# Performance work log

Measured on AMD Instinct MI355X. Metric: run time of the kernel, lower is better.

## Reference

```python
import jax, jax.numpy as jnp
import numpy as np

B, N, D, F = 8, 2048, 768, 768

def setup_inputs() -> dict:
    key = jax.random.key(0)
    k1, k2, k3, k4 = jax.random.split(key, 4)
    inputs = jax.random.normal(k1, (B, N, D), dtype=jnp.float32)
    # keras 'uniform' initializer: RandomUniform(-0.05, 0.05)
    W_q = jax.random.uniform(k2, (D, F), dtype=jnp.float32, minval=-0.05, maxval=0.05)
    W_k = jax.random.uniform(k3, (D, F), dtype=jnp.float32, minval=-0.05, maxval=0.05)
    W_v = jax.random.uniform(k4, (D, D), dtype=jnp.float32, minval=-0.05, maxval=0.05)
    return {"inputs": inputs, "W_q": W_q, "W_k": W_k, "W_v": W_v}

def reference(inputs, W_q, W_k, W_v):
    # q,k: [B,N,F]; v: [B,N,D]
    q = jnp.einsum('bnd,df->bnf', inputs, W_q)
    k = jnp.einsum('bnd,df->bnf', inputs, W_k)
    v = jnp.einsum('bnd,de->bne', inputs, W_v)
    scores = jnp.einsum('bnf,bmf->bnm', q, k)  # [B,N,N], no 1/sqrt(d) scaling (as in source)
    attn = jax.nn.softmax(scores, axis=-1)
    out = jnp.einsum('bnm,bmd->bnd', attn, v)
    return out
```

## Files before the change

### kernel.cpp

```cpp
#include <hip/hip_runtime.h>


typedef __attribute__((ext_vector_type(8))) _Float16 half8;
typedef __attribute__((ext_vector_type(4))) _Float16 half4v;
typedef __attribute__((ext_vector_type(4))) float floatx4;

__device__ __forceinline__ _Float16 f2h(float f) { return (_Float16)f; }
#define MFMA16 __builtin_amdgcn_mfma_f32_16x16x32_f16

__global__ __launch_bounds__(256) void cast_x_kernel(const float* __restrict__ X,
    _Float16* __restrict__ Xh) {
  size_t idx = (size_t)blockIdx.x * 256 + threadIdx.x;
  for (size_t o8 = idx; o8 < 1572864u; o8 += 524288u) {
    size_t o = o8 * 8;
    float4 a = *(const float4*)(X + o);
    float4 b = *(const float4*)(X + o + 4);
    *(half8*)(Xh + o) = (half8){f2h(a.x), f2h(a.y), f2h(a.z), f2h(a.w),
                                f2h(b.x), f2h(b.y), f2h(b.z), f2h(b.w)};
  }
}

__global__ __launch_bounds__(256) void mm_small_kernel(const float* __restrict__ Wq,
    const float* __restrict__ Wk, _Float16* __restrict__ Mh) {
  __shared__ _Float16 As[128][72];
  __shared__ _Float16 Bs[128][72];
  int bn = blockIdx.x, bm = blockIdx.y;
  int tid = threadIdx.x, lane = tid & 63, wave = tid >> 6;
  int wm = wave >> 1, wn = wave & 1;
  int l15 = lane & 15, quad = lane >> 4;
  floatx4 acc[16];
  for (int i = 0; i < 16; i++) acc[i] = (floatx4){0.f, 0.f, 0.f, 0.f};
  for (int k0 = 0; k0 < 768; k0 += 64) {
    __syncthreads();
    for (int i = 0; i < 8; i++) {
      int f = i * 256 + tid;
      int row = f >> 4, c4 = (f & 15) << 2;
      float4 va = *(const float4*)(Wq + (size_t)(bm * 128 + row) * 768 + k0 + c4);
      *(half4v*)&As[row][c4] = (half4v){f2h(va.x), f2h(va.y), f2h(va.z), f2h(va.w)};
      float4 vb = *(const float4*)(Wk + (size_t)(bn * 128 + row) * 768 + k0 + c4);
      *(half4v*)&Bs[row][c4] = (half4v){f2h(vb.x), f2h(vb.y), f2h(vb.z), f2h(vb.w)};
    }
    __syncthreads();
    for (int kk = 0; kk < 2; kk++) {
      half8 a[4], b[4];
      for (int mt = 0; mt < 4; mt++) a[mt] = *(half8*)&As[wm * 64 + mt * 16 + l15][kk * 32 + quad * 8];
      for (int nt = 0; nt < 4; nt++) b[nt] = *(half8*)&Bs[wn * 64 + nt * 16 + l15][kk * 32 + quad * 8];
      for (int mt = 0; mt < 4; mt++)
        for (int nt = 0; nt < 4; nt++)
          acc[mt * 4 + nt] = MFMA16(a[mt], b[nt], acc[mt * 4 + nt], 0, 0, 0);
    }
  }
  for (int mt = 0; mt < 4; mt++)
    for (int nt = 0; nt < 4; nt++) {
      int e = bn * 128 + wn * 64 + nt * 16 + l15;
      for (int r = 0; r < 4; r++) {
        int d = bm * 128 + wm * 64 + mt * 16 + quad * 4 + r;
        Mh[(size_t)d * 768 + e] = f2h(acc[mt * 4 + nt][r]);
      }
    }
}

__global__ void pack_wv_kernel(const float* __restrict__ Wv, _Float16* __restrict__ WvT) {
  __shared__ float tile[32][33];
  int k0 = blockIdx.x * 32;
  int n0 = blockIdx.y * 32;
  int tx = threadIdx.x, ty = threadIdx.y;
  for (int yy = ty; yy < 32; yy += 8)
    tile[yy][tx] = Wv[(size_t)(k0 + yy) * 768 + n0 + tx];
  __syncthreads();
  for (int yy = ty; yy < 32; yy += 8)
    WvT[(size_t)(n0 + yy) * 768 + k0 + tx] = f2h(tile[tx][yy]);
}

__global__ __launch_bounds__(256) void proj_h_kernel(const _Float16* __restrict__ Xh,
    const _Float16* __restrict__ Mh, _Float16* __restrict__ H) {
  __shared__ _Float16 As[128][72];
  __shared__ _Float16 Bs[128][72];
  int bn = blockIdx.x, bm = blockIdx.y;
  int tid = threadIdx.x, lane = tid & 63, wave = tid >> 6;
  int wm = wave >> 1, wn = wave & 1;
  int l15 = lane & 15, quad = lane >> 4;
  floatx4 acc[16];
  for (int i = 0; i < 16; i++) acc[i] = (floatx4){0.f, 0.f, 0.f, 0.f};
  for (int k0 = 0; k0 < 768; k0 += 64) {
    __syncthreads();
    for (int i = 0; i < 4; i++) {
      int f = i * 256 + tid;
      int row = f >> 3, c8 = (f & 7) << 3;
      *(half8*)&As[row][c8] = *(const half8*)(Xh + (size_t)(bm * 128 + row) * 768 + k0 + c8);
      *(half8*)&Bs[row][c8] = *(const half8*)(Mh + (size_t)(bn * 128 + row) * 768 + k0 + c8);
    }
    __syncthreads();
    for (int kk = 0; kk < 2; kk++) {
      half8 a[4], b[4];
      for (int mt = 0; mt < 4; mt++) a[mt] = *(half8*)&As[wm * 64 + mt * 16 + l15][kk * 32 + quad * 8];
      for (int nt = 0; nt < 4; nt++) b[nt] = *(half8*)&Bs[wn * 64 + nt * 16 + l15][kk * 32 + quad * 8];
      for (int mt = 0; mt < 4; mt++)
        for (int nt = 0; nt < 4; nt++)
          acc[mt * 4 + nt] = MFMA16(a[mt], b[nt], acc[mt * 4 + nt], 0, 0, 0);
    }
  }
  for (int mt = 0; mt < 4; mt++)
    for (int nt = 0; nt < 4; nt++) {
      int col = bn * 128 + wn * 64 + nt * 16 + l15;
      for (int r = 0; r < 4; r++) {
        int row = bm * 128 + wm * 64 + mt * 16 + quad * 4 + r;
        H[(size_t)row * 768 + col] = f2h(acc[mt * 4 + nt][r]);
      }
    }
}

__global__ __launch_bounds__(256) void proj_v_kernel(const _Float16* __restrict__ Xh,
    const _Float16* __restrict__ WvT, _Float16* __restrict__ Vt) {
  __shared__ _Float16 As[128][72];
  __shared__ _Float16 Bs[128][72];
  int bn = blockIdx.x, bm = blockIdx.y;
  int tid = threadIdx.x, lane = tid & 63, wave = tid >> 6;
  int wm = wave >> 1, wn = wave & 1;
  int l15 = lane & 15, quad = lane >> 4;
  floatx4 acc[16];
  for (int i = 0; i < 16; i++) acc[i] = (floatx4){0.f, 0.f, 0.f, 0.f};
  for (int k0 = 0; k0 < 768; k0 += 64) {
    __syncthreads();
    for (int i = 0; i < 4; i++) {
      int f = i * 256 + tid;
      int row = f >> 3, c8 = (f & 7) << 3;
      *(half8*)&As[row][c8] = *(const half8*)(Xh + (size_t)(bm * 128 + row) * 768 + k0 + c8);
      *(half8*)&Bs[row][c8] = *(const half8*)(WvT + (size_t)(bn * 128 + row) * 768 + k0 + c8);
    }
    __syncthreads();
    for (int kk = 0; kk < 2; kk++) {
      half8 a[4], b[4];
      for (int mt = 0; mt < 4; mt++) a[mt] = *(half8*)&As[wm * 64 + mt * 16 + l15][kk * 32 + quad * 8];
      for (int nt = 0; nt < 4; nt++) b[nt] = *(half8*)&Bs[wn * 64 + nt * 16 + l15][kk * 32 + quad * 8];
      for (int mt = 0; mt < 4; mt++)
        for (int nt = 0; nt < 4; nt++)
          acc[mt * 4 + nt] = MFMA16(a[mt], b[nt], acc[mt * 4 + nt], 0, 0, 0);
    }
  }
  for (int mt = 0; mt < 4; mt++)
    for (int nt = 0; nt < 4; nt++) {
      int d = bn * 128 + wn * 64 + nt * 16 + l15;
      int tok0 = bm * 128 + wm * 64 + mt * 16 + quad * 4;
      int bb = tok0 >> 11, ntok = tok0 & 2047;
      half4v p;
      for (int r = 0; r < 4; r++) p[r] = f2h(acc[mt * 4 + nt][r]);
      *(half4v*)(Vt + (size_t)(bb * 768 + d) * 2048 + ntok) = p;
    }
}

__global__ __launch_bounds__(512, 2) void attn_kernel(const _Float16* __restrict__ H,
    const float* __restrict__ X, const _Float16* __restrict__ Vt, float* __restrict__ out) {
  __shared__ _Float16 Qs[64][776];
  __shared__ _Float16 Pl[64][136];
  __shared__ float pm[8][64];
  __shared__ float psum[8][64];
  __shared__ float m_run[64], l_run[64], gmax[64], galpha[64];

  int id = blockIdx.x;
  int b = id & 7;
  int q0 = (id >> 3) * 64;
  int tid = threadIdx.x;
  int lane = tid & 63, w = tid >> 6;
  int l15 = lane & 15, quad = lane >> 4;

  if (tid < 64) { m_run[tid] = -1e30f; l_run[tid] = 0.f; }

  floatx4 accO[24];
  for (int i = 0; i < 24; i++) accO[i] = (floatx4){0.f, 0.f, 0.f, 0.f};

  const float*    Xq    = X + (size_t)(b * 2048 + q0) * 768;
  const _Float16* Hbase = H + (size_t)(b * 2048) * 768;
  const _Float16* Vbase = Vt + (size_t)b * 768 * 2048;

  for (int i = 0; i < 12; i++) {
    int f = i * 512 + tid;
    int row = f / 96, c8 = (f % 96) * 8;
    float4 a = *(const float4*)(Xq + (size_t)row * 768 + c8);
    float4 c = *(const float4*)(Xq + (size_t)row * 768 + c8 + 4);
    *(half8*)&Qs[row][c8] = (half8){f2h(a.x), f2h(a.y), f2h(a.z), f2h(a.w),
                                    f2h(c.x), f2h(c.y), f2h(c.z), f2h(c.w)};
  }
  __syncthreads();

  for (int m0 = 0; m0 < 2048; m0 += 128) {
    floatx4 sa[4];
    #pragma unroll
    for (int ss = 0; ss < 4; ss++) sa[ss] = (floatx4){0.f, 0.f, 0.f, 0.f};
    const _Float16* Kr = Hbase + (size_t)(m0 + w * 16 + l15) * 768 + quad * 8;
    half8 kpre[8];
    #pragma unroll
    for (int i = 0; i < 8; i++) kpre[i] = *(const half8*)(Kr + i * 32);
    #pragma unroll
    for (int kb = 0; kb < 24; kb++) {
      half8 kcur = kpre[kb & 7];
      int nxt = (kb + 8 < 24) ? (kb + 8) * 32 : 0;
      kpre[kb & 7] = *(const half8*)(Kr + nxt);
      #pragma unroll
      for (int ss = 0; ss < 4; ss++) {
        half8 qa = *(half8*)&Qs[ss * 16 + l15][kb * 32 + quad * 8];
        sa[ss] = MFMA16(qa, kcur, sa[ss], 0, 0, 0);
      }
    }
    const _Float16* vb0 = Vbase + (size_t)(w * 96 + l15) * 2048 + m0 + quad * 8;
    half8 vpre[8];
    #pragma unroll
    for (int i = 0; i < 8; i++) {
      int nks = i / 6, nnt = i % 6;
      vpre[i] = *(const half8*)(vb0 + (size_t)nnt * 16 * 2048 + nks * 32);
    }

    float mv[16];
    #pragma unroll
    for (int i = 0; i < 16; i++) mv[i] = sa[i >> 2][i & 3];
    #pragma unroll
    for (int mask = 1; mask <= 8; mask <<= 1)
      #pragma unroll
      for (int i = 0; i < 16; i++) mv[i] = fmaxf(mv[i], __shfl_xor(mv[i], mask));
    if (l15 == 0) {
      #pragma unroll
      for (int i = 0; i < 16; i++) pm[w][(i >> 2) * 16 + quad * 4 + (i & 3)] = mv[i];
    }
    __syncthreads();
    if (tid < 64) {
      float mo = m_run[tid];
      float mn = mo;
      #pragma unroll
      for (int w2 = 0; w2 < 8; w2++) mn = fmaxf(mn, pm[w2][tid]);
      gmax[tid] = mn;
      galpha[tid] = __expf(mo - mn);
      m_run[tid] = mn;
    }
    __syncthreads();
    float pr[16], al[16];
    #pragma unroll
    for (int i = 0; i < 16; i++) {
      int ss = i >> 2, r = i & 3;
      int row = ss * 16 + quad * 4 + r;
      float mn = gmax[row];
      al[i] = galpha[row];
      float p = __expf(sa[ss][r] - mn);
      pr[i] = p;
      Pl[row][w * 16 + l15] = f2h(p);
    }
    #pragma unroll
    for (int mask = 1; mask <= 8; mask <<= 1)
      #pragma unroll
      for (int i = 0; i < 16; i++) pr[i] += __shfl_xor(pr[i], mask);
    if (l15 == 0) {
      #pragma unroll
      for (int i = 0; i < 16; i++) psum[w][(i >> 2) * 16 + quad * 4 + (i & 3)] = pr[i];
    }
    #pragma unroll
    for (int nt = 0; nt < 6; nt++)
      #pragma unroll
      for (int i = 0; i < 16; i++)
        accO[nt * 4 + (i >> 2)][i & 3] *= al[i];
    __syncthreads();
    if (tid < 64) {
      float s = 0.f;
      #pragma unroll
      for (int w2 = 0; w2 < 8; w2++) s += psum[w2][tid];
      l_run[tid] = l_run[tid] * galpha[tid] + s;
    }
    #pragma unroll
    for (int ks = 0; ks < 4; ks++) {
      half8 pa[4];
      #pragma unroll
      for (int ss = 0; ss < 4; ss++) pa[ss] = *(half8*)&Pl[ss * 16 + l15][ks * 32 + quad * 8];
      #pragma unroll
      for (int nt = 0; nt < 6; nt++) {
        int idx = ks * 6 + nt;
        half8 vcur = vpre[idx & 7];
        int nidx = idx + 8;
        int nks = (nidx < 24) ? nidx / 6 : 0;
        int nnt = (nidx < 24) ? nidx % 6 : 0;
        vpre[idx & 7] = *(const half8*)(vb0 + (size_t)nnt * 16 * 2048 + nks * 32);
        #pragma unroll
        for (int ss = 0; ss < 4; ss++)
          accO[nt * 4 + ss] = MFMA16(pa[ss], vcur, accO[nt * 4 + ss], 0, 0, 0);
      }
    }
  }
  __syncthreads();
  float il[16];
  #pragma unroll
  for (int i = 0; i < 16; i++) {
    int row = (i >> 2) * 16 + quad * 4 + (i & 3);
    il[i] = 1.f / l_run[row];
  }
  #pragma unroll
  for (int nt = 0; nt < 6; nt++)
    #pragma unroll
    for (int ss = 0; ss < 4; ss++) {
      int d = w * 96 + nt * 16 + l15;
      #pragma unroll
      for (int r = 0; r < 4; r++) {
        int row = q0 + ss * 16 + quad * 4 + r;
        out[(size_t)(b * 2048 + row) * 768 + d] = accO[nt * 4 + ss][r] * il[ss * 4 + r];
      }
    }
}

extern "C" void kernel_launch(void* const* d_in, const int* in_sizes, int n_in,
                              void* d_out, int out_size, void* d_ws, size_t ws_size,
                              hipStream_t stream) {
  (void)in_sizes; (void)n_in; (void)out_size; (void)ws_size;
  const float* X  = (const float*)d_in[0];
  const float* Wq = (const float*)d_in[1];
  const float* Wk = (const float*)d_in[2];
  const float* Wv = (const float*)d_in[3];
  float* out = (float*)d_out;

  char* ws = (char*)d_ws;
  _Float16* H  = (_Float16*)ws;
  _Float16* Vt = (_Float16*)(ws + 25165824);

  _Float16* Mh  = (_Float16*)d_out;
  _Float16* WvT = (_Float16*)((char*)d_out + 2359296);
  _Float16* Xh  = (_Float16*)((char*)d_out + 4194304);

  cast_x_kernel<<<2048, 256, 0, stream>>>(X, Xh);
  mm_small_kernel<<<dim3(6, 6), 256, 0, stream>>>(Wq, Wk, Mh);
  pack_wv_kernel<<<dim3(24, 24), dim3(32, 8), 0, stream>>>(Wv, WvT);
  proj_h_kernel<<<dim3(6, 128), 256, 0, stream>>>(Xh, Mh, H);
  proj_v_kernel<<<dim3(6, 128), 256, 0, stream>>>(Xh, WvT, Vt);
  attn_kernel<<<256, 512, 0, stream>>>(H, X, Vt, out);
}
```

Baseline: 447.7 us.

## Double-buffer projection GEMM tiles and prefetch next K/V block in attention

The two projection GEMMs now stage their tiles through a pair of shared-memory buffers, loading the next K-slice from global memory into registers while MFMAs run on the current one, which cuts one barrier per iteration. In the attention kernel, the K and V register prefetch rings now reach across block boundaries: the tail prefetches pull the first chunks of the next 128-key block rather than reloading the current one, and the prologue loads are hoisted out of the loop. The aim is to hide global load latency at block starts. The cost is twice the LDS in the projection kernels and some redundant wrap-around loads on the last block.

```diff
diff --git a/kernel.cpp b/kernel.cpp
--- a/kernel.cpp
+++ b/kernel.cpp
@@ -74,30 +74,61 @@
 
 __global__ __launch_bounds__(256) void proj_h_kernel(const _Float16* __restrict__ Xh,
     const _Float16* __restrict__ Mh, _Float16* __restrict__ H) {
-  __shared__ _Float16 As[128][72];
-  __shared__ _Float16 Bs[128][72];
+  __shared__ _Float16 As[2][128][72];
+  __shared__ _Float16 Bs[2][128][72];
   int bn = blockIdx.x, bm = blockIdx.y;
   int tid = threadIdx.x, lane = tid & 63, wave = tid >> 6;
   int wm = wave >> 1, wn = wave & 1;
   int l15 = lane & 15, quad = lane >> 4;
   floatx4 acc[16];
   for (int i = 0; i < 16; i++) acc[i] = (floatx4){0.f, 0.f, 0.f, 0.f};
-  for (int k0 = 0; k0 < 768; k0 += 64) {
-    __syncthreads();
-    for (int i = 0; i < 4; i++) {
-      int f = i * 256 + tid;
-      int row = f >> 3, c8 = (f & 7) << 3;
-      *(half8*)&As[row][c8] = *(const half8*)(Xh + (size_t)(bm * 128 + row) * 768 + k0 + c8);
-      *(half8*)&Bs[row][c8] = *(const half8*)(Mh + (size_t)(bn * 128 + row) * 768 + k0 + c8);
-    }
-    __syncthreads();
+  half8 ra[4], rb[4];
+  #pragma unroll
+  for (int i = 0; i < 4; i++) {
+    int f = i * 256 + tid, row = f >> 3, c8 = (f & 7) << 3;
+    ra[i] = *(const half8*)(Xh + (size_t)(bm * 128 + row) * 768 + c8);
+    rb[i] = *(const half8*)(Mh + (size_t)(bn * 128 + row) * 768 + c8);
+  }
+  #pragma unroll
+  for (int i = 0; i < 4; i++) {
+    int f = i * 256 + tid, row = f >> 3, c8 = (f & 7) << 3;
+    *(half8*)&As[0][row][c8] = ra[i];
+    *(half8*)&Bs[0][row][c8] = rb[i];
+  }
+  __syncthreads();
+  int cur = 0;
+  for (int t = 0; t < 12; t++) {
+    if (t < 11) {
+      int k0 = (t + 1) * 64;
+      #pragma unroll
+      for (int i = 0; i < 4; i++) {
+        int f = i * 256 + tid, row = f >> 3, c8 = (f & 7) << 3;
+        ra[i] = *(const half8*)(Xh + (size_t)(bm * 128 + row) * 768 + k0 + c8);
+        rb[i] = *(const half8*)(Mh + (size_t)(bn * 128 + row) * 768 + k0 + c8);
+      }
+    }
+    #pragma unroll
     for (int kk = 0; kk < 2; kk++) {
       half8 a[4], b[4];
-      for (int mt = 0; mt < 4; mt++) a[mt] = *(half8*)&As[wm * 64 + mt * 16 + l15][kk * 32 + quad * 8];
-      for (int nt = 0; nt < 4; nt++) b[nt] = *(half8*)&Bs[wn * 64 + nt * 16 + l15][kk * 32 + quad * 8];
+      #pragma unroll
+      for (int mt = 0; mt < 4; mt++) a[mt] = *(half8*)&As[cur][wm * 64 + mt * 16 + l15][kk * 32 + quad * 8];
+      #pragma unroll
+      for (int nt = 0; nt < 4; nt++) b[nt] = *(half8*)&Bs[cur][wn * 64 + nt * 16 + l15][kk * 32 + quad * 8];
+      #pragma unroll
       for (int mt = 0; mt < 4; mt++)
+        #pragma unroll
         for (int nt = 0; nt < 4; nt++)
           acc[mt * 4 + nt] = MFMA16(a[mt], b[nt], acc[mt * 4 + nt], 0, 0, 0);
+    }
+    if (t < 11) {
+      #pragma unroll
+      for (int i = 0; i < 4; i++) {
+        int f = i * 256 + tid, row = f >> 3, c8 = (f & 7) << 3;
+        *(half8*)&As[cur ^ 1][row][c8] = ra[i];
+        *(half8*)&Bs[cur ^ 1][row][c8] = rb[i];
+      }
+      __syncthreads();
+      cur ^= 1;
     }
   }
   for (int mt = 0; mt < 4; mt++)
@@ -112,30 +143,61 @@
 
 __global__ __launch_bounds__(256) void proj_v_kernel(const _Float16* __restrict__ Xh,
     const _Float16* __restrict__ WvT, _Float16* __restrict__ Vt) {
-  __shared__ _Float16 As[128][72];
-  __shared__ _Float16 Bs[128][72];
+  __shared__ _Float16 As[2][128][72];
+  __shared__ _Float16 Bs[2][128][72];
   int bn = blockIdx.x, bm = blockIdx.y;
   int tid = threadIdx.x, lane = tid & 63, wave = tid >> 6;
   int wm = wave >> 1, wn = wave & 1;
   int l15 = lane & 15, quad = lane >> 4;
   floatx4 acc[16];
   for (int i = 0; i < 16; i++) acc[i] = (floatx4){0.f, 0.f, 0.f, 0.f};
-  for (int k0 = 0; k0 < 768; k0 += 64) {
-    __syncthreads();
-    for (int i = 0; i < 4; i++) {
-      int f = i * 256 + tid;
-      int row = f >> 3, c8 = (f & 7) << 3;
-      *(half8*)&As[row][c8] = *(const half8*)(Xh + (size_t)(bm * 128 + row) * 768 + k0 + c8);
-      *(half8*)&Bs[row][c8] = *(const half8*)(WvT + (size_t)(bn * 128 + row) * 768 + k0 + c8);
-    }
-    __syncthreads();
+  half8 ra[4], rb[4];
+  #pragma unroll
+  for (int i = 0; i < 4; i++) {
+    int f = i * 256 + tid, row = f >> 3, c8 = (f & 7) << 3;
+    ra[i] = *(const half8*)(Xh + (size_t)(bm * 128 + row) * 768 + c8);
+    rb[i] = *(const half8*)(WvT + (size_t)(bn * 128 + row) * 768 + c8);
+  }
+  #pragma unroll
+  for (int i = 0; i < 4; i++) {
+    int f = i * 256 + tid, row = f >> 3, c8 = (f & 7) << 3;
+    *(half8*)&As[0][row][c8] = ra[i];
+    *(half8*)&Bs[0][row][c8] = rb[i];
+  }
+  __syncthreads();
+  int cur = 0;
+  for (int t = 0; t < 12; t++) {
+    if (t < 11) {
+      int k0 = (t + 1) * 64;
+      #pragma unroll
+      for (int i = 0; i < 4; i++) {
+        int f = i * 256 + tid, row = f >> 3, c8 = (f & 7) << 3;
+        ra[i] = *(const half8*)(Xh + (size_t)(bm * 128 + row) * 768 + k0 + c8);
+        rb[i] = *(const half8*)(WvT + (size_t)(bn * 128 + row) * 768 + k0 + c8);
+      }
+    }
+    #pragma unroll
     for (int kk = 0; kk < 2; kk++) {
       half8 a[4], b[4];
-      for (int mt = 0; mt < 4; mt++) a[mt] = *(half8*)&As[wm * 64 + mt * 16 + l15][kk * 32 + quad * 8];
-      for (int nt = 0; nt < 4; nt++) b[nt] = *(half8*)&Bs[wn * 64 + nt * 16 + l15][kk * 32 + quad * 8];
+      #pragma unroll
+      for (int mt = 0; mt < 4; mt++) a[mt] = *(half8*)&As[cur][wm * 64 + mt * 16 + l15][kk * 32 + quad * 8];
+      #pragma unroll
+      for (int nt = 0; nt < 4; nt++) b[nt] = *(half8*)&Bs[cur][wn * 64 + nt * 16 + l15][kk * 32 + quad * 8];
+      #pragma unroll
       for (int mt = 0; mt < 4; mt++)
+        #pragma unroll
         for (int nt = 0; nt < 4; nt++)
           acc[mt * 4 + nt] = MFMA16(a[mt], b[nt], acc[mt * 4 + nt], 0, 0, 0);
+    }
+    if (t < 11) {
+      #pragma unroll
+      for (int i = 0; i < 4; i++) {
+        int f = i * 256 + tid, row = f >> 3, c8 = (f & 7) << 3;
+        *(half8*)&As[cur ^ 1][row][c8] = ra[i];
+        *(half8*)&Bs[cur ^ 1][row][c8] = rb[i];
+      }
+      __syncthreads();
+      cur ^= 1;
     }
   }
   for (int mt = 0; mt < 4; mt++)
@@ -172,6 +234,8 @@
   const float*    Xq    = X + (size_t)(b * 2048 + q0) * 768;
   const _Float16* Hbase = H + (size_t)(b * 2048) * 768;
   const _Float16* Vbase = Vt + (size_t)b * 768 * 2048;
+  const _Float16* KrBase = Hbase + (size_t)(w * 16 + l15) * 768 + quad * 8;
+  const _Float16* VrBase = Vbase + (size_t)(w * 96 + l15) * 2048 + quad * 8;
 
   for (int i = 0; i < 12; i++) {
     int f = i * 512 + tid;
@@ -181,34 +245,37 @@
     *(half8*)&Qs[row][c8] = (half8){f2h(a.x), f2h(a.y), f2h(a.z), f2h(a.w),
                                     f2h(c.x), f2h(c.y), f2h(c.z), f2h(c.w)};
   }
+
+  half8 kpre[8], vpre[8];
+  #pragma unroll
+  for (int i = 0; i < 8; i++) kpre[i] = *(const half8*)(KrBase + i * 32);
+  #pragma unroll
+  for (int i = 0; i < 8; i++)
+    vpre[i] = *(const half8*)(VrBase + (size_t)(i % 6) * 16 * 2048 + (i / 6) * 32);
   __syncthreads();
 
   for (int m0 = 0; m0 < 2048; m0 += 128) {
+    int mn = (m0 + 128) & 2047;
+    const _Float16* Kr  = KrBase + (size_t)m0 * 768;
+    const _Float16* KrN = KrBase + (size_t)mn * 768;
+    const _Float16* vb0 = VrBase + m0;
+    const _Float16* vbN = VrBase + mn;
     floatx4 sa[4];
     #pragma unroll
     for (int ss = 0; ss < 4; ss++) sa[ss] = (floatx4){0.f, 0.f, 0.f, 0.f};
-    const _Float16* Kr = Hbase + (size_t)(m0 + w * 16 + l15) * 768 + quad * 8;
-    half8 kpre[8];
-    #pragma unroll
-    for (int i = 0; i < 8; i++) kpre[i] = *(const half8*)(Kr + i * 32);
     #pragma unroll
     for (int kb = 0; kb < 24; kb++) {
       half8 kcur = kpre[kb & 7];
-      int nxt = (kb + 8 < 24) ? (kb + 8) * 32 : 0;
-      kpre[kb & 7] = *(const half8*)(Kr + nxt);
+      if (kb + 8 < 24)
+        kpre[kb & 7] = *(const half8*)(Kr + (kb + 8) * 32);
+      else
+        kpre[kb & 7] = *(const half8*)(KrN + (kb + 8 - 24) * 32);
       #pragma unroll
       for (int ss = 0; ss < 4; ss++) {
         half8 qa = *(half8*)&Qs[ss * 16 + l15][kb * 32 + quad * 8];
         sa[ss] = MFMA16(qa, kcur, sa[ss], 0, 0, 0);
       }
     }
-    const _Float16* vb0 = Vbase + (size_t)(w * 96 + l15) * 2048 + m0 + quad * 8;
-    half8 vpre[8];
-    #pragma unroll
-    for (int i = 0; i < 8; i++) {
-      int nks = i / 6, nnt = i % 6;
-      vpre[i] = *(const half8*)(vb0 + (size_t)nnt * 16 * 2048 + nks * 32);
-    }
 
     float mv[16];
     #pragma unroll
@@ -224,12 +291,12 @@
     __syncthreads();
     if (tid < 64) {
       float mo = m_run[tid];
-      float mn = mo;
-      #pragma unroll
-      for (int w2 = 0; w2 < 8; w2++) mn = fmaxf(mn, pm[w2][tid]);
-      gmax[tid] = mn;
-      galpha[tid] = __expf(mo - mn);
-      m_run[tid] = mn;
+      float mn2 = mo;
+      #pragma unroll
+      for (int w2 = 0; w2 < 8; w2++) mn2 = fmaxf(mn2, pm[w2][tid]);
+      gmax[tid] = mn2;
+      galpha[tid] = __expf(mo - mn2);
+      m_run[tid] = mn2;
     }
     __syncthreads();
     float pr[16], al[16];
@@ -237,9 +304,9 @@
     for (int i = 0; i < 16; i++) {
       int ss = i >> 2, r = i & 3;
       int row = ss * 16 + quad * 4 + r;
-      float mn = gmax[row];
+      float mn2 = gmax[row];
       al[i] = galpha[row];
-      float p = __expf(sa[ss][r] - mn);
+      float p = __expf(sa[ss][r] - mn2);
       pr[i] = p;
       Pl[row][w * 16 + l15] = f2h(p);
     }
@@ -273,9 +340,10 @@
         int idx = ks * 6 + nt;
         half8 vcur = vpre[idx & 7];
         int nidx = idx + 8;
-        int nks = (nidx < 24) ? nidx / 6 : 0;
-        int nnt = (nidx < 24) ? nidx % 6 : 0;
-        vpre[idx & 7] = *(const half8*)(vb0 + (size_t)nnt * 16 * 2048 + nks * 32);
+        if (nidx < 24)
+          vpre[idx & 7] = *(const half8*)(vb0 + (size_t)(nidx % 6) * 16 * 2048 + (nidx / 6) * 32);
+        else
+          vpre[idx & 7] = *(const half8*)(vbN + (size_t)((nidx - 24) % 6) * 16 * 2048 + ((nidx - 24) / 6) * 32);
         #pragma unroll
         for (int ss = 0; ss < 4; ss++)
           accO[nt * 4 + ss] = MFMA16(pa[ss], vcur, accO[nt * 4 + ss], 0, 0, 0);
```

Result: no change. 454.4 us (+1.5%).

## Switch attention to 32x32 MFMA tiles and register-prefetch projection GEMM tiles

Applied to the files above, without the earlier changes.

The attention kernel now uses 32x32x16 MFMA instructions. Waves are rearranged into a 2x4 grid over query rows and key columns, and QK^T is accumulated into two alternating accumulators to break the dependency chain. The softmax reductions are adapted to the 32-lane layout. The projection GEMMs gain register double-buffering: the next K tile is loaded from global memory while MFMAs run on the current shared tile. The aim is fewer LDS reads per MFMA, plus latency hiding in the projections, at the cost of more register pressure.

```diff
diff --git a/kernel.cpp b/kernel.cpp
--- a/kernel.cpp
+++ b/kernel.cpp
@@ -4,9 +4,12 @@
 typedef __attribute__((ext_vector_type(8))) _Float16 half8;
 typedef __attribute__((ext_vector_type(4))) _Float16 half4v;
 typedef __attribute__((ext_vector_type(4))) float floatx4;
+typedef __attribute__((ext_vector_type(16))) float floatx16;
 
 __device__ __forceinline__ _Float16 f2h(float f) { return (_Float16)f; }
 #define MFMA16 __builtin_amdgcn_mfma_f32_16x16x32_f16
+#define MFMA32 __builtin_amdgcn_mfma_f32_32x32x16_f16
+#define CROW(r) (((r) & 3) + 8 * ((r) >> 2))
 
 __global__ __launch_bounds__(256) void cast_x_kernel(const float* __restrict__ X,
     _Float16* __restrict__ Xh) {
@@ -82,23 +85,44 @@
   int l15 = lane & 15, quad = lane >> 4;
   floatx4 acc[16];
   for (int i = 0; i < 16; i++) acc[i] = (floatx4){0.f, 0.f, 0.f, 0.f};
-  for (int k0 = 0; k0 < 768; k0 += 64) {
-    __syncthreads();
+  half8 ra[4], rb[4];
+  #pragma unroll
+  for (int i = 0; i < 4; i++) {
+    int f = i * 256 + tid, row = f >> 3, c8 = (f & 7) << 3;
+    ra[i] = *(const half8*)(Xh + (size_t)(bm * 128 + row) * 768 + c8);
+    rb[i] = *(const half8*)(Mh + (size_t)(bn * 128 + row) * 768 + c8);
+  }
+  for (int t = 0; t < 12; t++) {
+    #pragma unroll
     for (int i = 0; i < 4; i++) {
-      int f = i * 256 + tid;
-      int row = f >> 3, c8 = (f & 7) << 3;
-      *(half8*)&As[row][c8] = *(const half8*)(Xh + (size_t)(bm * 128 + row) * 768 + k0 + c8);
-      *(half8*)&Bs[row][c8] = *(const half8*)(Mh + (size_t)(bn * 128 + row) * 768 + k0 + c8);
-    }
-    __syncthreads();
+      int f = i * 256 + tid, row = f >> 3, c8 = (f & 7) << 3;
+      *(half8*)&As[row][c8] = ra[i];
+      *(half8*)&Bs[row][c8] = rb[i];
+    }
+    __syncthreads();
+    if (t < 11) {
+      int k0 = (t + 1) * 64;
+      #pragma unroll
+      for (int i = 0; i < 4; i++) {
+        int f = i * 256 + tid, row = f >> 3, c8 = (f & 7) << 3;
+        ra[i] = *(const half8*)(Xh + (size_t)(bm * 128 + row) * 768 + k0 + c8);
+        rb[i] = *(const half8*)(Mh + (size_t)(bn * 128 + row) * 768 + k0 + c8);
+      }
+    }
+    #pragma unroll
     for (int kk = 0; kk < 2; kk++) {
       half8 a[4], b[4];
+      #pragma unroll
       for (int mt = 0; mt < 4; mt++) a[mt] = *(half8*)&As[wm * 64 + mt * 16 + l15][kk * 32 + quad * 8];
+      #pragma unroll
       for (int nt = 0; nt < 4; nt++) b[nt] = *(half8*)&Bs[wn * 64 + nt * 16 + l15][kk * 32 + quad * 8];
+      #pragma unroll
       for (int mt = 0; mt < 4; mt++)
+        #pragma unroll
         for (int nt = 0; nt < 4; nt++)
           acc[mt * 4 + nt] = MFMA16(a[mt], b[nt], acc[mt * 4 + nt], 0, 0, 0);
     }
+    __syncthreads();
   }
   for (int mt = 0; mt < 4; mt++)
     for (int nt = 0; nt < 4; nt++) {
@@ -120,23 +144,44 @@
   int l15 = lane & 15, quad = lane >> 4;
   floatx4 acc[16];
   for (int i = 0; i < 16; i++) acc[i] = (floatx4){0.f, 0.f, 0.f, 0.f};
-  for (int k0 = 0; k0 < 768; k0 += 64) {
-    __syncthreads();
+  half8 ra[4], rb[4];
+  #pragma unroll
+  for (int i = 0; i < 4; i++) {
+    int f = i * 256 + tid, row = f >> 3, c8 = (f & 7) << 3;
+    ra[i] = *(const half8*)(Xh + (size_t)(bm * 128 + row) * 768 + c8);
+    rb[i] = *(const half8*)(WvT + (size_t)(bn * 128 + row) * 768 + c8);
+  }
+  for (int t = 0; t < 12; t++) {
+    #pragma unroll
     for (int i = 0; i < 4; i++) {
-      int f = i * 256 + tid;
-      int row = f >> 3, c8 = (f & 7) << 3;
-      *(half8*)&As[row][c8] = *(const half8*)(Xh + (size_t)(bm * 128 + row) * 768 + k0 + c8);
-      *(half8*)&Bs[row][c8] = *(const half8*)(WvT + (size_t)(bn * 128 + row) * 768 + k0 + c8);
-    }
-    __syncthreads();
+      int f = i * 256 + tid, row = f >> 3, c8 = (f & 7) << 3;
+      *(half8*)&As[row][c8] = ra[i];
+      *(half8*)&Bs[row][c8] = rb[i];
+    }
+    __syncthreads();
+    if (t < 11) {
+      int k0 = (t + 1) * 64;
+      #pragma unroll
+      for (int i = 0; i < 4; i++) {
+        int f = i * 256 + tid, row = f >> 3, c8 = (f & 7) << 3;
+        ra[i] = *(const half8*)(Xh + (size_t)(bm * 128 + row) * 768 + k0 + c8);
+        rb[i] = *(const half8*)(WvT + (size_t)(bn * 128 + row) * 768 + k0 + c8);
+      }
+    }
+    #pragma unroll
     for (int kk = 0; kk < 2; kk++) {
       half8 a[4], b[4];
+      #pragma unroll
       for (int mt = 0; mt < 4; mt++) a[mt] = *(half8*)&As[wm * 64 + mt * 16 + l15][kk * 32 + quad * 8];
+      #pragma unroll
       for (int nt = 0; nt < 4; nt++) b[nt] = *(half8*)&Bs[wn * 64 + nt * 16 + l15][kk * 32 + quad * 8];
+      #pragma unroll
       for (int mt = 0; mt < 4; mt++)
+        #pragma unroll
         for (int nt = 0; nt < 4; nt++)
           acc[mt * 4 + nt] = MFMA16(a[mt], b[nt], acc[mt * 4 + nt], 0, 0, 0);
     }
+    __syncthreads();
   }
   for (int mt = 0; mt < 4; mt++)
     for (int nt = 0; nt < 4; nt++) {
@@ -153,8 +198,8 @@
     const float* __restrict__ X, const _Float16* __restrict__ Vt, float* __restrict__ out) {
   __shared__ _Float16 Qs[64][776];
   __shared__ _Float16 Pl[64][136];
-  __shared__ float pm[8][64];
-  __shared__ float psum[8][64];
+  __shared__ float pm2[4][64];
+  __shared__ float ps2[4][64];
   __shared__ float m_run[64], l_run[64], gmax[64], galpha[64];
 
   int id = blockIdx.x;
@@ -162,16 +207,20 @@
   int q0 = (id >> 3) * 64;
   int tid = threadIdx.x;
   int lane = tid & 63, w = tid >> 6;
-  int l15 = lane & 15, quad = lane >> 4;
+  int l31 = lane & 31, hi = lane >> 5;
+  int wq = w & 1, wk = w >> 1;
 
   if (tid < 64) { m_run[tid] = -1e30f; l_run[tid] = 0.f; }
 
-  floatx4 accO[24];
-  for (int i = 0; i < 24; i++) accO[i] = (floatx4){0.f, 0.f, 0.f, 0.f};
+  floatx16 accO[6];
+  for (int i = 0; i < 6; i++)
+    for (int r = 0; r < 16; r++) accO[i][r] = 0.f;
 
   const float*    Xq    = X + (size_t)(b * 2048 + q0) * 768;
   const _Float16* Hbase = H + (size_t)(b * 2048) * 768;
   const _Float16* Vbase = Vt + (size_t)b * 768 * 2048;
+  const _Float16* KrB   = Hbase + (size_t)(wk * 32 + l31) * 768 + hi * 8;
+  const _Float16* VrB   = Vbase + (size_t)(w * 96 + l31) * 2048 + hi * 8;
 
   for (int i = 0; i < 12; i++) {
     int f = i * 512 + tid;
@@ -184,122 +233,118 @@
   __syncthreads();
 
   for (int m0 = 0; m0 < 2048; m0 += 128) {
-    floatx4 sa[4];
-    #pragma unroll
-    for (int ss = 0; ss < 4; ss++) sa[ss] = (floatx4){0.f, 0.f, 0.f, 0.f};
-    const _Float16* Kr = Hbase + (size_t)(m0 + w * 16 + l15) * 768 + quad * 8;
+    const _Float16* Kr = KrB + (size_t)m0 * 768;
+    const _Float16* Vr = VrB + m0;
+    floatx16 s0, s1;
+    #pragma unroll
+    for (int r = 0; r < 16; r++) { s0[r] = 0.f; s1[r] = 0.f; }
     half8 kpre[8];
     #pragma unroll
-    for (int i = 0; i < 8; i++) kpre[i] = *(const half8*)(Kr + i * 32);
-    #pragma unroll
-    for (int kb = 0; kb < 24; kb++) {
+    for (int i = 0; i < 8; i++) kpre[i] = *(const half8*)(Kr + i * 16);
+    #pragma unroll
+    for (int kb = 0; kb < 48; kb++) {
       half8 kcur = kpre[kb & 7];
-      int nxt = (kb + 8 < 24) ? (kb + 8) * 32 : 0;
+      int nxt = (kb + 8 < 48) ? (kb + 8) * 16 : 0;
       kpre[kb & 7] = *(const half8*)(Kr + nxt);
-      #pragma unroll
-      for (int ss = 0; ss < 4; ss++) {
-        half8 qa = *(half8*)&Qs[ss * 16 + l15][kb * 32 + quad * 8];
-        sa[ss] = MFMA16(qa, kcur, sa[ss], 0, 0, 0);
-      }
-    }
-    const _Float16* vb0 = Vbase + (size_t)(w * 96 + l15) * 2048 + m0 + quad * 8;
+      half8 qa = *(half8*)&Qs[wq * 32 + l31][kb * 16 + hi * 8];
+      if (kb & 1) s1 = MFMA32(qa, kcur, s1, 0, 0, 0);
+      else        s0 = MFMA32(qa, kcur, s0, 0, 0, 0);
+    }
+    float sav[16];
+    #pragma unroll
+    for (int r = 0; r < 16; r++) sav[r] = s0[r] + s1[r];
     half8 vpre[8];
     #pragma unroll
-    for (int i = 0; i < 8; i++) {
-      int nks = i / 6, nnt = i % 6;
-      vpre[i] = *(const half8*)(vb0 + (size_t)nnt * 16 * 2048 + nks * 32);
-    }
+    for (int i = 0; i < 8; i++)
+      vpre[i] = *(const half8*)(Vr + (size_t)(i % 3) * 32 * 2048 + (i / 3) * 16);
 
     float mv[16];
     #pragma unroll
-    for (int i = 0; i < 16; i++) mv[i] = sa[i >> 2][i & 3];
-    #pragma unroll
-    for (int mask = 1; mask <= 8; mask <<= 1)
-      #pragma unroll
-      for (int i = 0; i < 16; i++) mv[i] = fmaxf(mv[i], __shfl_xor(mv[i], mask));
-    if (l15 == 0) {
-      #pragma unroll
-      for (int i = 0; i < 16; i++) pm[w][(i >> 2) * 16 + quad * 4 + (i & 3)] = mv[i];
+    for (int r = 0; r < 16; r++) mv[r] = sav[r];
+    #pragma unroll
+    for (int mask = 1; mask <= 16; mask <<= 1)
+      #pragma unroll
+      for (int r = 0; r < 16; r++) mv[r] = fmaxf(mv[r], __shfl_xor(mv[r], mask));
+    if (l31 == 0) {
+      #pragma unroll
+      for (int r = 0; r < 16; r++) pm2[wk][wq * 32 + CROW(r) + 4 * hi] = mv[r];
     }
     __syncthreads();
     if (tid < 64) {
       float mo = m_run[tid];
       float mn = mo;
       #pragma unroll
-      for (int w2 = 0; w2 < 8; w2++) mn = fmaxf(mn, pm[w2][tid]);
+      for (int kg = 0; kg < 4; kg++) mn = fmaxf(mn, pm2[kg][tid]);
       gmax[tid] = mn;
       galpha[tid] = __expf(mo - mn);
       m_run[tid] = mn;
     }
     __syncthreads();
-    float pr[16], al[16];
-    #pragma unroll
-    for (int i = 0; i < 16; i++) {
-      int ss = i >> 2, r = i & 3;
-      int row = ss * 16 + quad * 4 + r;
-      float mn = gmax[row];
-      al[i] = galpha[row];
-      float p = __expf(sa[ss][r] - mn);
-      pr[i] = p;
-      Pl[row][w * 16 + l15] = f2h(p);
-    }
-    #pragma unroll
-    for (int mask = 1; mask <= 8; mask <<= 1)
-      #pragma unroll
-      for (int i = 0; i < 16; i++) pr[i] += __shfl_xor(pr[i], mask);
-    if (l15 == 0) {
-      #pragma unroll
-      for (int i = 0; i < 16; i++) psum[w][(i >> 2) * 16 + quad * 4 + (i & 3)] = pr[i];
-    }
-    #pragma unroll
-    for (int nt = 0; nt < 6; nt++)
-      #pragma unroll
-      for (int i = 0; i < 16; i++)
-        accO[nt * 4 + (i >> 2)][i & 3] *= al[i];
+    float pr[16];
+    #pragma unroll
+    for (int r = 0; r < 16; r++) {
+      int row = wq * 32 + CROW(r) + 4 * hi;
+      float p = __expf(sav[r] - gmax[row]);
+      pr[r] = p;
+      Pl[row][wk * 32 + l31] = f2h(p);
+    }
+    #pragma unroll
+    for (int mask = 1; mask <= 16; mask <<= 1)
+      #pragma unroll
+      for (int r = 0; r < 16; r++) pr[r] += __shfl_xor(pr[r], mask);
+    if (l31 == 0) {
+      #pragma unroll
+      for (int r = 0; r < 16; r++) ps2[wk][wq * 32 + CROW(r) + 4 * hi] = pr[r];
+    }
+    #pragma unroll
+    for (int r = 0; r < 16; r++) {
+      int cr = CROW(r) + 4 * hi;
+      float a0 = galpha[cr], a1 = galpha[32 + cr];
+      accO[0][r] *= a0; accO[1][r] *= a0; accO[2][r] *= a0;
+      accO[3][r] *= a1; accO[4][r] *= a1; accO[5][r] *= a1;
+    }
     __syncthreads();
     if (tid < 64) {
       float s = 0.f;
       #pragma unroll
-      for (int w2 = 0; w2 < 8; w2++) s += psum[w2][tid];
+      for (int kg = 0; kg < 4; kg++) s += ps2[kg][tid];
       l_run[tid] = l_run[tid] * galpha[tid] + s;
     }
     #pragma unroll
-    for (int ks = 0; ks < 4; ks++) {
-      half8 pa[4];
-      #pragma unroll
-      for (int ss = 0; ss < 4; ss++) pa[ss] = *(half8*)&Pl[ss * 16 + l15][ks * 32 + quad * 8];
-      #pragma unroll
-      for (int nt = 0; nt < 6; nt++) {
-        int idx = ks * 6 + nt;
+    for (int kc = 0; kc < 8; kc++) {
+      half8 pa0 = *(half8*)&Pl[l31][kc * 16 + hi * 8];
+      half8 pa1 = *(half8*)&Pl[32 + l31][kc * 16 + hi * 8];
+      #pragma unroll
+      for (int dt = 0; dt < 3; dt++) {
+        int idx = kc * 3 + dt;
         half8 vcur = vpre[idx & 7];
         int nidx = idx + 8;
-        int nks = (nidx < 24) ? nidx / 6 : 0;
-        int nnt = (nidx < 24) ? nidx % 6 : 0;
-        vpre[idx & 7] = *(const half8*)(vb0 + (size_t)nnt * 16 * 2048 + nks * 32);
-        #pragma unroll
-        for (int ss = 0; ss < 4; ss++)
-          accO[nt * 4 + ss] = MFMA16(pa[ss], vcur, accO[nt * 4 + ss], 0, 0, 0);
+        int kc2 = (nidx < 24) ? nidx / 3 : 0;
+        int dt2 = (nidx < 24) ? nidx % 3 : 0;
+        vpre[idx & 7] = *(const half8*)(Vr + (size_t)dt2 * 32 * 2048 + kc2 * 16);
+        accO[dt]     = MFMA32(pa0, vcur, accO[dt], 0, 0, 0);
+        accO[3 + dt] = MFMA32(pa1, vcur, accO[3 + dt], 0, 0, 0);
       }
     }
   }
   __syncthreads();
-  float il[16];
+  float il0[16], il1[16];
   #pragma unroll
-  for (int i = 0; i < 16; i++) {
-    int row = (i >> 2) * 16 + quad * 4 + (i & 3);
-    il[i] = 1.f / l_run[row];
+  for (int r = 0; r < 16; r++) {
+    int cr = CROW(r) + 4 * hi;
+    il0[r] = 1.f / l_run[cr];
+    il1[r] = 1.f / l_run[32 + cr];
   }
   #pragma unroll
-  for (int nt = 0; nt < 6; nt++)
-    #pragma unroll
-    for (int ss = 0; ss < 4; ss++) {
-      int d = w * 96 + nt * 16 + l15;
-      #pragma unroll
-      for (int r = 0; r < 4; r++) {
-        int row = q0 + ss * 16 + quad * 4 + r;
-        out[(size_t)(b * 2048 + row) * 768 + d] = accO[nt * 4 + ss][r] * il[ss * 4 + r];
-      }
-    }
+  for (int dt = 0; dt < 3; dt++) {
+    int d = w * 96 + dt * 32 + l31;
+    #pragma unroll
+    for (int r = 0; r < 16; r++) {
+      int cr = CROW(r) + 4 * hi;
+      out[(size_t)(b * 2048 + q0 + cr) * 768 + d]      = accO[dt][r] * il0[r];
+      out[(size_t)(b * 2048 + q0 + 32 + cr) * 768 + d] = accO[3 + dt][r] * il1[r];
+    }
+  }
 }
 
 extern "C" void kernel_launch(void* const* d_in, const int* in_sizes, int n_in,
```

Result: slower. 515.4 us (+15.1%).

## Merge prep kernels and H/V projections, add register-prefetch double buffering

Applied to the files above, without the earlier changes.

Folds the three preprocessing kernels (X cast, Wq·Wk^T product, Wv transpose) into one launch that dispatches on block index. It also folds the H and V projection GEMMs into one grid of 12x128 blocks. The projection loop now prefetches the next K tile into registers while MFMAs run on the current LDS tile, and the loops are fully unrolled. The aim is to cut launch overhead and tail gaps between small kernels and to hide global load latency. The cost is more register pressure and divergent block roles within one kernel.

```diff
diff --git a/kernel.cpp b/kernel.cpp
--- a/kernel.cpp
+++ b/kernel.cpp
@@ -8,145 +8,145 @@
 __device__ __forceinline__ _Float16 f2h(float f) { return (_Float16)f; }
 #define MFMA16 __builtin_amdgcn_mfma_f32_16x16x32_f16
 
-__global__ __launch_bounds__(256) void cast_x_kernel(const float* __restrict__ X,
-    _Float16* __restrict__ Xh) {
-  size_t idx = (size_t)blockIdx.x * 256 + threadIdx.x;
-  for (size_t o8 = idx; o8 < 1572864u; o8 += 524288u) {
-    size_t o = o8 * 8;
-    float4 a = *(const float4*)(X + o);
-    float4 b = *(const float4*)(X + o + 4);
-    *(half8*)(Xh + o) = (half8){f2h(a.x), f2h(a.y), f2h(a.z), f2h(a.w),
-                                f2h(b.x), f2h(b.y), f2h(b.z), f2h(b.w)};
-  }
-}
-
-__global__ __launch_bounds__(256) void mm_small_kernel(const float* __restrict__ Wq,
-    const float* __restrict__ Wk, _Float16* __restrict__ Mh) {
+__global__ __launch_bounds__(256) void prep_kernel(const float* __restrict__ X,
+    const float* __restrict__ Wq, const float* __restrict__ Wk,
+    const float* __restrict__ Wv, _Float16* __restrict__ Xh,
+    _Float16* __restrict__ Mh, _Float16* __restrict__ WvT) {
   __shared__ _Float16 As[128][72];
   __shared__ _Float16 Bs[128][72];
-  int bn = blockIdx.x, bm = blockIdx.y;
+  __shared__ float tileF[32][33];
+  int id = blockIdx.x;
+  int tid = threadIdx.x;
+  if (id < 2048) {
+    size_t idx = (size_t)id * 256 + tid;
+    for (size_t o8 = idx; o8 < 1572864u; o8 += 524288u) {
+      size_t o = o8 * 8;
+      float4 a = *(const float4*)(X + o);
+      float4 b = *(const float4*)(X + o + 4);
+      *(half8*)(Xh + o) = (half8){f2h(a.x), f2h(a.y), f2h(a.z), f2h(a.w),
+                                  f2h(b.x), f2h(b.y), f2h(b.z), f2h(b.w)};
+    }
+  } else if (id < 2624) {
+    int pid = id - 2048;
+    int k0 = (pid % 24) * 32, n0 = (pid / 24) * 32;
+    int tx = tid & 31, ty = tid >> 5;
+    for (int yy = ty; yy < 32; yy += 8)
+      tileF[yy][tx] = Wv[(size_t)(k0 + yy) * 768 + n0 + tx];
+    __syncthreads();
+    for (int yy = ty; yy < 32; yy += 8)
+      WvT[(size_t)(n0 + yy) * 768 + k0 + tx] = f2h(tileF[tx][yy]);
+  } else {
+    int pid = id - 2624;
+    int bn = pid % 6, bm = pid / 6;
+    int lane = tid & 63, wave = tid >> 6;
+    int wm = wave >> 1, wn = wave & 1;
+    int l15 = lane & 15, quad = lane >> 4;
+    floatx4 acc[16];
+    for (int i = 0; i < 16; i++) acc[i] = (floatx4){0.f, 0.f, 0.f, 0.f};
+    for (int k0 = 0; k0 < 768; k0 += 64) {
+      __syncthreads();
+      for (int i = 0; i < 8; i++) {
+        int f = i * 256 + tid;
+        int row = f >> 4, c4 = (f & 15) << 2;
+        float4 va = *(const float4*)(Wq + (size_t)(bm * 128 + row) * 768 + k0 + c4);
+        *(half4v*)&As[row][c4] = (half4v){f2h(va.x), f2h(va.y), f2h(va.z), f2h(va.w)};
+        float4 vb = *(const float4*)(Wk + (size_t)(bn * 128 + row) * 768 + k0 + c4);
+        *(half4v*)&Bs[row][c4] = (half4v){f2h(vb.x), f2h(vb.y), f2h(vb.z), f2h(vb.w)};
+      }
+      __syncthreads();
+      for (int kk = 0; kk < 2; kk++) {
+        half8 a[4], b[4];
+        for (int mt = 0; mt < 4; mt++) a[mt] = *(half8*)&As[wm * 64 + mt * 16 + l15][kk * 32 + quad * 8];
+        for (int nt = 0; nt < 4; nt++) b[nt] = *(half8*)&Bs[wn * 64 + nt * 16 + l15][kk * 32 + quad * 8];
+        for (int mt = 0; mt < 4; mt++)
+          for (int nt = 0; nt < 4; nt++)
+            acc[mt * 4 + nt] = MFMA16(a[mt], b[nt], acc[mt * 4 + nt], 0, 0, 0);
+      }
+    }
+    for (int mt = 0; mt < 4; mt++)
+      for (int nt = 0; nt < 4; nt++) {
+        int e = bn * 128 + wn * 64 + nt * 16 + l15;
+        for (int r = 0; r < 4; r++) {
+          int d = bm * 128 + wm * 64 + mt * 16 + quad * 4 + r;
+          Mh[(size_t)d * 768 + e] = f2h(acc[mt * 4 + nt][r]);
+        }
+      }
+  }
+}
+
+__global__ __launch_bounds__(256) void proj_kernel(const _Float16* __restrict__ Xh,
+    const _Float16* __restrict__ Mh, const _Float16* __restrict__ WvT,
+    _Float16* __restrict__ H, _Float16* __restrict__ Vt) {
+  __shared__ _Float16 As[128][72];
+  __shared__ _Float16 Bs[128][72];
+  int bnRaw = blockIdx.x, bm = blockIdx.y;
+  int isV = bnRaw >= 6;
+  int bn = isV ? bnRaw - 6 : bnRaw;
+  const _Float16* Bsrc = isV ? WvT : Mh;
   int tid = threadIdx.x, lane = tid & 63, wave = tid >> 6;
   int wm = wave >> 1, wn = wave & 1;
   int l15 = lane & 15, quad = lane >> 4;
   floatx4 acc[16];
   for (int i = 0; i < 16; i++) acc[i] = (floatx4){0.f, 0.f, 0.f, 0.f};
-  for (int k0 = 0; k0 < 768; k0 += 64) {
-    __syncthreads();
-    for (int i = 0; i < 8; i++) {
-      int f = i * 256 + tid;
-      int row = f >> 4, c4 = (f & 15) << 2;
-      float4 va = *(const float4*)(Wq + (size_t)(bm * 128 + row) * 768 + k0 + c4);
-      *(half4v*)&As[row][c4] = (half4v){f2h(va.x), f2h(va.y), f2h(va.z), f2h(va.w)};
-      float4 vb = *(const float4*)(Wk + (size_t)(bn * 128 + row) * 768 + k0 + c4);
-      *(half4v*)&Bs[row][c4] = (half4v){f2h(vb.x), f2h(vb.y), f2h(vb.z), f2h(vb.w)};
-    }
-    __syncthreads();
+  half8 ra[4], rb[4];
+  #pragma unroll
+  for (int i = 0; i < 4; i++) {
+    int f = i * 256 + tid, row = f >> 3, c8 = (f & 7) << 3;
+    ra[i] = *(const half8*)(Xh + (size_t)(bm * 128 + row) * 768 + c8);
+    rb[i] = *(const half8*)(Bsrc + (size_t)(bn * 128 + row) * 768 + c8);
+  }
+  for (int t = 0; t < 12; t++) {
+    #pragma unroll
+    for (int i = 0; i < 4; i++) {
+      int f = i * 256 + tid, row = f >> 3, c8 = (f & 7) << 3;
+      *(half8*)&As[row][c8] = ra[i];
+      *(half8*)&Bs[row][c8] = rb[i];
+    }
+    __syncthreads();
+    if (t < 11) {
+      int k0 = (t + 1) * 64;
+      #pragma unroll
+      for (int i = 0; i < 4; i++) {
+        int f = i * 256 + tid, row = f >> 3, c8 = (f & 7) << 3;
+        ra[i] = *(const half8*)(Xh + (size_t)(bm * 128 + row) * 768 + k0 + c8);
+        rb[i] = *(const half8*)(Bsrc + (size_t)(bn * 128 + row) * 768 + k0 + c8);
+      }
+    }
+    #pragma unroll
     for (int kk = 0; kk < 2; kk++) {
       half8 a[4], b[4];
+      #pragma unroll
       for (int mt = 0; mt < 4; mt++) a[mt] = *(half8*)&As[wm * 64 + mt * 16 + l15][kk * 32 + quad * 8];
+      #pragma unroll
       for (int nt = 0; nt < 4; nt++) b[nt] = *(half8*)&Bs[wn * 64 + nt * 16 + l15][kk * 32 + quad * 8];
+      #pragma unroll
       for (int mt = 0; mt < 4; mt++)
+        #pragma unroll
         for (int nt = 0; nt < 4; nt++)
           acc[mt * 4 + nt] = MFMA16(a[mt], b[nt], acc[mt * 4 + nt], 0, 0, 0);
     }
-  }
-  for (int mt = 0; mt < 4; mt++)
-    for (int nt = 0; nt < 4; nt++) {
-      int e = bn * 128 + wn * 64 + nt * 16 + l15;
-      for (int r = 0; r < 4; r++) {
-        int d = bm * 128 + wm * 64 + mt * 16 + quad * 4 + r;
-        Mh[(size_t)d * 768 + e] = f2h(acc[mt * 4 + nt][r]);
-      }
-    }
-}
-
-__global__ void pack_wv_kernel(const float* __restrict__ Wv, _Float16* __restrict__ WvT) {
-  __shared__ float tile[32][33];
-  int k0 = blockIdx.x * 32;
-  int n0 = blockIdx.y * 32;
-  int tx = threadIdx.x, ty = threadIdx.y;
-  for (int yy = ty; yy < 32; yy += 8)
-    tile[yy][tx] = Wv[(size_t)(k0 + yy) * 768 + n0 + tx];
-  __syncthreads();
-  for (int yy = ty; yy < 32; yy += 8)
-    WvT[(size_t)(n0 + yy) * 768 + k0 + tx] = f2h(tile[tx][yy]);
-}
-
-__global__ __launch_bounds__(256) void proj_h_kernel(const _Float16* __restrict__ Xh,
-    const _Float16* __restrict__ Mh, _Float16* __restrict__ H) {
-  __shared__ _Float16 As[128][72];
-  __shared__ _Float16 Bs[128][72];
-  int bn = blockIdx.x, bm = blockIdx.y;
-  int tid = threadIdx.x, lane = tid & 63, wave = tid >> 6;
-  int wm = wave >> 1, wn = wave & 1;
-  int l15 = lane & 15, quad = lane >> 4;
-  floatx4 acc[16];
-  for (int i = 0; i < 16; i++) acc[i] = (floatx4){0.f, 0.f, 0.f, 0.f};
-  for (int k0 = 0; k0 < 768; k0 += 64) {
-    __syncthreads();
-    for (int i = 0; i < 4; i++) {
-      int f = i * 256 + tid;
-      int row = f >> 3, c8 = (f & 7) << 3;
-      *(half8*)&As[row][c8] = *(const half8*)(Xh + (size_t)(bm * 128 + row) * 768 + k0 + c8);
-      *(half8*)&Bs[row][c8] = *(const half8*)(Mh + (size_t)(bn * 128 + row) * 768 + k0 + c8);
-    }
-    __syncthreads();
-    for (int kk = 0; kk < 2; kk++) {
-      half8 a[4], b[4];
-      for (int mt = 0; mt < 4; mt++) a[mt] = *(half8*)&As[wm * 64 + mt * 16 + l15][kk * 32 + quad * 8];
-      for (int nt = 0; nt < 4; nt++) b[nt] = *(half8*)&Bs[wn * 64 + nt * 16 + l15][kk * 32 + quad * 8];
-      for (int mt = 0; mt < 4; mt++)
-        for (int nt = 0; nt < 4; nt++)
-          acc[mt * 4 + nt] = MFMA16(a[mt], b[nt], acc[mt * 4 + nt], 0, 0, 0);
-    }
-  }
-  for (int mt = 0; mt < 4; mt++)
-    for (int nt = 0; nt < 4; nt++) {
-      int col = bn * 128 + wn * 64 + nt * 16 + l15;
-      for (int r = 0; r < 4; r++) {
-        int row = bm * 128 + wm * 64 + mt * 16 + quad * 4 + r;
-        H[(size_t)row * 768 + col] = f2h(acc[mt * 4 + nt][r]);
-      }
-    }
-}
-
-__global__ __launch_bounds__(256) void proj_v_kernel(const _Float16* __restrict__ Xh,
-    const _Float16* __restrict__ WvT, _Float16* __restrict__ Vt) {
-  __shared__ _Float16 As[128][72];
-  __shared__ _Float16 Bs[128][72];
-  int bn = blockIdx.x, bm = blockIdx.y;
-  int tid = threadIdx.x, lane = tid & 63, wave = tid >> 6;
-  int wm = wave >> 1, wn = wave & 1;
-  int l15 = lane & 15, quad = lane >> 4;
-  floatx4 acc[16];
-  for (int i = 0; i < 16; i++) acc[i] = (floatx4){0.f, 0.f, 0.f, 0.f};
-  for (int k0 = 0; k0 < 768; k0 += 64) {
-    __syncthreads();
-    for (int i = 0; i < 4; i++) {
-      int f = i * 256 + tid;
-      int row = f >> 3, c8 = (f & 7) << 3;
-      *(half8*)&As[row][c8] = *(const half8*)(Xh + (size_t)(bm * 128 + row) * 768 + k0 + c8);
-      *(half8*)&Bs[row][c8] = *(const half8*)(WvT + (size_t)(bn * 128 + row) * 768 + k0 + c8);
-    }
-    __syncthreads();
-    for (int kk = 0; kk < 2; kk++) {
-      half8 a[4], b[4];
-      for (int mt = 0; mt < 4; mt++) a[mt] = *(half8*)&As[wm * 64 + mt * 16 + l15][kk * 32 + quad * 8];
-      for (int nt = 0; nt < 4; nt++) b[nt] = *(half8*)&Bs[wn * 64 + nt * 16 + l15][kk * 32 + quad * 8];
-      for (int mt = 0; mt < 4; mt++)
-        for (int nt = 0; nt < 4; nt++)
-          acc[mt * 4 + nt] = MFMA16(a[mt], b[nt], acc[mt * 4 + nt], 0, 0, 0);
-    }
-  }
-  for (int mt = 0; mt < 4; mt++)
-    for (int nt = 0; nt < 4; nt++) {
-      int d = bn * 128 + wn * 64 + nt * 16 + l15;
-      int tok0 = bm * 128 + wm * 64 + mt * 16 + quad * 4;
-      int bb = tok0 >> 11, ntok = tok0 & 2047;
-      half4v p;
-      for (int r = 0; r < 4; r++) p[r] = f2h(acc[mt * 4 + nt][r]);
-      *(half4v*)(Vt + (size_t)(bb * 768 + d) * 2048 + ntok) = p;
-    }
+    __syncthreads();
+  }
+  if (!isV) {
+    for (int mt = 0; mt < 4; mt++)
+      for (int nt = 0; nt < 4; nt++) {
+        int col = bn * 128 + wn * 64 + nt * 16 + l15;
+        for (int r = 0; r < 4; r++) {
+          int row = bm * 128 + wm * 64 + mt * 16 + quad * 4 + r;
+          H[(size_t)row * 768 + col] = f2h(acc[mt * 4 + nt][r]);
+        }
+      }
+  } else {
+    for (int mt = 0; mt < 4; mt++)
+      for (int nt = 0; nt < 4; nt++) {
+        int d = bn * 128 + wn * 64 + nt * 16 + l15;
+        int tok0 = bm * 128 + wm * 64 + mt * 16 + quad * 4;
+        int bb = tok0 >> 11, ntok = tok0 & 2047;
+        half4v p;
+        for (int r = 0; r < 4; r++) p[r] = f2h(acc[mt * 4 + nt][r]);
+        *(half4v*)(Vt + (size_t)(bb * 768 + d) * 2048 + ntok) = p;
+      }
+  }
 }
 
 __global__ __launch_bounds__(512, 2) void attn_kernel(const _Float16* __restrict__ H,
@@ -320,10 +320,7 @@
   _Float16* WvT = (_Float16*)((char*)d_out + 2359296);
   _Float16* Xh  = (_Float16*)((char*)d_out + 4194304);
 
-  cast_x_kernel<<<2048, 256, 0, stream>>>(X, Xh);
-  mm_small_kernel<<<dim3(6, 6), 256, 0, stream>>>(Wq, Wk, Mh);
-  pack_wv_kernel<<<dim3(24, 24), dim3(32, 8), 0, stream>>>(Wv, WvT);
-  proj_h_kernel<<<dim3(6, 128), 256, 0, stream>>>(Xh, Mh, H);
-  proj_v_kernel<<<dim3(6, 128), 256, 0, stream>>>(Xh, WvT, Vt);
+  prep_kernel<<<2660, 256, 0, stream>>>(X, Wq, Wk, Wv, Xh, Mh, WvT);
+  proj_kernel<<<dim3(12, 128), 256, 0, stream>>>(Xh, Mh, WvT, H, Vt);
   attn_kernel<<<256, 512, 0, stream>>>(H, X, Vt, out);
 }
```

Result: faster. 428.4 us (-4.3%).
